# Optimization experiments

Measured on AMD Instinct MI355X. Metric: run time of the kernel, lower is better.

Reference implementation:

```python
import jax, jax.numpy as jnp
import numpy as np


def setup_inputs() -> dict:
    key = jax.random.key(0)
    ks = jax.random.split(key, 8)
    B, N, E_PER, M = 8, 50000, 1000000, 2048  # graphs, nodes/graph, edges/graph, decision neurons
    BN, E = B * N, B * E_PER
    x = jax.random.normal(ks[0], (BN, 1), dtype=jnp.float32)
    edge_weight = jax.random.uniform(ks[1], (E,), minval=0.0, maxval=10.0, dtype=jnp.float32)
    # within-graph edges with PyG-style batch offsets
    offs = jnp.repeat(jnp.arange(B, dtype=jnp.int32) * N, E_PER)
    src = jax.random.randint(ks[2], (E,), 0, N, dtype=jnp.int32) + offs
    dst = jax.random.randint(ks[3], (E,), 0, N, dtype=jnp.int32) + offs
    # indices where decision_making_vector == 1 (static for jit)
    dm_indices = jnp.sort(jax.random.randint(ks[4], (M,), 0, N, dtype=jnp.int32))
    fc_w = jax.random.normal(ks[5], (1, 1), dtype=jnp.float32)
    fc_b = jax.random.normal(ks[6], (1,), dtype=jnp.float32)
    return {"x": x, "edge_weight": edge_weight, "src": src, "dst": dst,
            "dm_indices": dm_indices, "fc_w": fc_w, "fc_b": fc_b,
            "batch_size": 8, "num_passes": 3}


def reference(x, edge_weight, src, dst, dm_indices, fc_w, fc_b, batch_size, num_passes):
    # log1p edge transform
    ew = jnp.log1p(edge_weight)  # [E]
    BN = x.shape[0]
    N = BN // batch_size
    h = x  # [BN, 1]
    # TrainableEdgeConv: num_passes rounds of scatter-add message passing + per-graph L2 norm over nodes
    for _ in range(num_passes):
        msgs = h[src] * ew[:, None]                      # [E, 1] gather + scale
        h = jax.ops.segment_sum(msgs, dst, num_segments=BN)  # scatter-add to dst
        hb = h.reshape(batch_size, N, -1)
        hb = hb / jnp.linalg.norm(hb, axis=1, keepdims=True)  # x / x.norm(dim=1)
        h = hb.reshape(BN, -1)
    # decision_making_mask: select decision neurons
    v = h.reshape(batch_size, N, -1)[:, dm_indices, 0]  # [B, M]
    # normalize_non_zero: per-graph mean/std over nonzero entries (unbiased std, like scatter_std)
    mask = v != 0
    cnt = mask.sum(axis=1, keepdims=True).astype(v.dtype)
    mean = jnp.where(mask, v, 0.0).sum(axis=1, keepdims=True) / cnt
    var = jnp.where(mask, (v - mean) ** 2, 0.0).sum(axis=1, keepdims=True) / jnp.maximum(cnt - 1.0, 1.0)
    std = jnp.sqrt(var) + 1e-5
    v = jnp.where(mask, (v - mean) / std, v)
    # mean pool over decision neurons, Linear(1,1), relu, squeeze -> [B]
    pooled = v.mean(axis=1)  # [B]
    out = pooled * fc_w[0, 0] + fc_b[0]
    return jax.nn.relu(out)
```

## Files before the change

kernel.cpp:

```cpp
#include <hip/hip_runtime.h>
#include <math.h>

#define GB    8
#define GN    50000
#define EPG   1000000
#define EDGES (GB*EPG)
#define NP    3

#define BW     4096
#define NBUCK  13
#define NBINS  (GB*NBUCK)
#define CAP    89088
#define CPB    20
#define STRIPE 4000
#define NQ     (STRIPE/4)
#define NBLKH  (EDGES/STRIPE)
#define BPG    (EPG/STRIPE)
#define SRCMASK 0x7FFFFu


__global__ void z_k(int* __restrict__ gcur, float* __restrict__ nsq,
                    float4* __restrict__ a, float4* __restrict__ b,
                    float4* __restrict__ c) {
  int i = blockIdx.x * 256 + threadIdx.x;
  float4 z = {0.f, 0.f, 0.f, 0.f};
  if (i < (GB * GN) / 4) { a[i] = z; b[i] = z; c[i] = z; }
  if (blockIdx.x == 0) {
    if (threadIdx.x < NBINS) gcur[threadIdx.x] = 0;
    if (threadIdx.x < GB) nsq[threadIdx.x] = 0.f;
  }
}

__global__ __launch_bounds__(256) void fscatter_k(
    const int* __restrict__ src, const int* __restrict__ dst,
    const float* __restrict__ ew, int* __restrict__ gcur,
    uint2* __restrict__ recs) {
  __shared__ int lh[NBINS];
  __shared__ int lb[NBINS];
  if (threadIdx.x < NBINS) lh[threadIdx.x] = 0;
  __syncthreads();
  int blk = blockIdx.x;
  int s0 = blk * STRIPE;
  int g = blk / BPG;
  int base = g * GN, gb = g * NBUCK;
  const int4* d4 = (const int4*)(dst + s0);
  const int4* s4 = (const int4*)(src + s0);
  const float4* w4 = (const float4*)(ew + s0);

  int rk[16];
#pragma unroll
  for (int u = 0; u < 4; ++u) {
    int q = threadIdx.x + 256 * u;
    if (q < NQ) {
      int4 d = d4[q];
      rk[4 * u + 0] = atomicAdd(&lh[gb + ((d.x - base) >> 12)], 1);
      rk[4 * u + 1] = atomicAdd(&lh[gb + ((d.y - base) >> 12)], 1);
      rk[4 * u + 2] = atomicAdd(&lh[gb + ((d.z - base) >> 12)], 1);
      rk[4 * u + 3] = atomicAdd(&lh[gb + ((d.w - base) >> 12)], 1);
    }
  }
  __syncthreads();
  if (threadIdx.x < NBINS) {
    int c = lh[threadIdx.x];
    lb[threadIdx.x] = c ? atomicAdd(&gcur[threadIdx.x], c) : 0;
  }
  __syncthreads();
#pragma unroll
  for (int u = 0; u < 4; ++u) {
    int q = threadIdx.x + 256 * u;
    if (q < NQ) {
      int4 d = d4[q]; int4 s = s4[q]; float4 w = w4[q];
      int dv[4] = {d.x, d.y, d.z, d.w};
      int sv[4] = {s.x, s.y, s.z, s.w};
      float wv[4] = {w.x, w.y, w.z, w.w};
#pragma unroll
      for (int k = 0; k < 4; ++k) {
        int dl = dv[k] - base;
        int bin = gb + (dl >> 12);
        int r = dl & (BW - 1);
        size_t pos = (size_t)bin * CAP + lb[bin] + rk[4 * u + k];
        recs[pos] = make_uint2(((unsigned)r << 19) | (unsigned)sv[k],
                               __float_as_uint(log1pf(wv[k])));
      }
    }
  }
}

__global__ __launch_bounds__(256) void accum_k(
    const uint2* __restrict__ recs, const int* __restrict__ cnt,
    const float* __restrict__ hin, float* __restrict__ hout) {
  __shared__ float acc[BW];
  int c = blockIdx.x;
  int bin = blockIdx.y;
  float4 z = {0.f, 0.f, 0.f, 0.f};
  float4* a4 = (float4*)acc;
  for (int i = threadIdx.x; i < BW / 4; i += 256) a4[i] = z;
  int len = cnt[bin];
  int chunk = ((len + CPB - 1) / CPB + 1) & ~1;
  int lo = c * chunk;
  int hi = lo + chunk;
  if (lo > len) lo = len;
  if (hi > len) hi = len;
  const uint2* rb = recs + (size_t)bin * CAP;
  __syncthreads();
  int rem = hi - lo;
  if (rem < 0) rem = 0;
  int np = rem >> 1;
  const uint4* rp = (const uint4*)(rb + lo);
  int p = threadIdx.x;
  for (; p + 256 < np; p += 512) {
    uint4 r0 = rp[p];
    uint4 r1 = rp[p + 256];
    float a0 = hin[r0.x & SRCMASK] * __uint_as_float(r0.y);
    float a1 = hin[r0.z & SRCMASK] * __uint_as_float(r0.w);
    float a2 = hin[r1.x & SRCMASK] * __uint_as_float(r1.y);
    float a3 = hin[r1.z & SRCMASK] * __uint_as_float(r1.w);
    atomicAdd(&acc[r0.x >> 19], a0);
    atomicAdd(&acc[r0.z >> 19], a1);
    atomicAdd(&acc[r1.x >> 19], a2);
    atomicAdd(&acc[r1.z >> 19], a3);
  }
  if (p < np) {
    uint4 r0 = rp[p];
    atomicAdd(&acc[r0.x >> 19], hin[r0.x & SRCMASK] * __uint_as_float(r0.y));
    atomicAdd(&acc[r0.z >> 19], hin[r0.z & SRCMASK] * __uint_as_float(r0.w));
  }
  if ((rem & 1) && threadIdx.x == 0) {
    uint2 a = rb[hi - 1];
    atomicAdd(&acc[a.x >> 19], hin[a.x & SRCMASK] * __uint_as_float(a.y));
  }
  __syncthreads();
  int g = bin / NBUCK, bucket = bin - g * NBUCK;
  int sw = GN - bucket * BW; if (sw > BW) sw = BW;
  float* ho = hout + (size_t)g * GN + (size_t)bucket * BW;
  for (int i = threadIdx.x; i < sw; i += 256) {
    float v = acc[i];
    if (v != 0.f) unsafeAtomicAdd(&ho[i], v);
  }
}

__global__ void nsq_k(const float4* __restrict__ h4, float* __restrict__ nsq) {
  __shared__ float sm[GB];
  if (threadIdx.x < GB) sm[threadIdx.x] = 0.f;
  __syncthreads();
  int n4 = blockIdx.x * 256 + threadIdx.x;
  if (n4 < (GB * GN) / 4) {
    float4 t = h4[n4];
    int g = (n4 * 4) / GN;
    atomicAdd(&sm[g], t.x * t.x + t.y * t.y + t.z * t.z + t.w * t.w);
  }
  __syncthreads();
  if (threadIdx.x < GB && sm[threadIdx.x] != 0.f)
    unsafeAtomicAdd(&nsq[threadIdx.x], sm[threadIdx.x]);
}


__global__ void init_k(const float* __restrict__ x, float* __restrict__ h_cur,
                       float* __restrict__ h_next, float* __restrict__ norms,
                       int BN, int n_norms) {
  int i = blockIdx.x * blockDim.x + threadIdx.x;
  int stride = gridDim.x * blockDim.x;
  for (int j = i; j < BN; j += stride) { h_cur[j] = x[j]; h_next[j] = 0.f; }
  if (i < n_norms) norms[i] = 0.f;
}

__global__ void edge_k(const int* __restrict__ src, const int* __restrict__ dst,
                       const float* __restrict__ ew, const float* __restrict__ h_in,
                       float* __restrict__ h_out, int E4, int E) {
  int i = blockIdx.x * blockDim.x + threadIdx.x;
  int stride = gridDim.x * blockDim.x;
  const int4* s4 = (const int4*)src;
  const int4* d4 = (const int4*)dst;
  const float4* w4 = (const float4*)ew;
  for (int j = i; j < E4; j += stride) {
    int4 s = s4[j]; int4 d = d4[j]; float4 w = w4[j];
    unsafeAtomicAdd(&h_out[d.x], h_in[s.x] * log1pf(w.x));
    unsafeAtomicAdd(&h_out[d.y], h_in[s.y] * log1pf(w.y));
    unsafeAtomicAdd(&h_out[d.z], h_in[s.z] * log1pf(w.z));
    unsafeAtomicAdd(&h_out[d.w], h_in[s.w] * log1pf(w.w));
  }
  for (int j = E4 * 4 + i; j < E; j += stride)
    unsafeAtomicAdd(&h_out[dst[j]], h_in[src[j]] * log1pf(ew[j]));
}

__global__ void norm_k(const float* __restrict__ h, float* __restrict__ norms, int N) {
  int g = blockIdx.y;
  const float* hg = h + (size_t)g * N;
  float s = 0.f;
  for (int j = blockIdx.x * blockDim.x + threadIdx.x; j < N; j += gridDim.x * blockDim.x) {
    float v = hg[j]; s += v * v;
  }
  __shared__ float sm[4];
  for (int o = 32; o > 0; o >>= 1) s += __shfl_down(s, o, 64);
  if ((threadIdx.x & 63) == 0) sm[threadIdx.x >> 6] = s;
  __syncthreads();
  if (threadIdx.x == 0) {
    float t = 0.f;
    for (int w = 0; w < (int)(blockDim.x >> 6); ++w) t += sm[w];
    unsafeAtomicAdd(&norms[g], t);
  }
}

__global__ void scale_k(const float* __restrict__ norms, float* __restrict__ h_next,
                        float* __restrict__ h_cur, int N) {
  int g = blockIdx.y;
  float inv = 1.0f / sqrtf(norms[g]);
  size_t off = (size_t)g * N;
  for (int j = blockIdx.x * blockDim.x + threadIdx.x; j < N; j += gridDim.x * blockDim.x) {
    h_cur[off + j] = h_next[off + j] * inv;
    h_next[off + j] = 0.f;
  }
}

__device__ __forceinline__ float blk_red(float t, float* sm, int nw) {
  for (int o = 32; o > 0; o >>= 1) t += __shfl_down(t, o, 64);
  if ((threadIdx.x & 63) == 0) sm[threadIdx.x >> 6] = t;
  __syncthreads();
  float r = 0.f;
  for (int w = 0; w < nw; ++w) r += sm[w];
  __syncthreads();
  return r;
}

__global__ void final_k(const float* __restrict__ h, const float* __restrict__ nsq,
                        const int* __restrict__ dm,
                        const float* __restrict__ fc_w, const float* __restrict__ fc_b,
                        float* __restrict__ out, int N, int M) {
  extern __shared__ float v[];
  __shared__ float sm[16];
  int b = blockIdx.x;
  int nw = blockDim.x >> 6;
  float inv = nsq ? 1.0f / sqrtf(nsq[b]) : 1.0f;
  const float* hb = h + (size_t)b * N;
  for (int m = threadIdx.x; m < M; m += blockDim.x) v[m] = hb[dm[m]] * inv;
  __syncthreads();

  float cnt = 0.f, sum = 0.f;
  for (int m = threadIdx.x; m < M; m += blockDim.x) {
    float xv = v[m];
    if (xv != 0.f) { cnt += 1.f; sum += xv; }
  }
  float totalSum = blk_red(sum, sm, nw);
  float totalCnt = blk_red(cnt, sm, nw);
  float mean = totalCnt > 0.f ? totalSum / totalCnt : 0.f;

  float ssq = 0.f;
  for (int m = threadIdx.x; m < M; m += blockDim.x) {
    float xv = v[m];
    if (xv != 0.f) { float d = xv - mean; ssq += d * d; }
  }
  float totalSsq = blk_red(ssq, sm, nw);

  float denom = totalCnt - 1.f;
  if (denom < 1.f) denom = 1.f;
  float stdv = sqrtf(totalSsq / denom) + 1e-5f;

  float ps = 0.f;
  for (int m = threadIdx.x; m < M; m += blockDim.x) {
    float xv = v[m];
    if (xv != 0.f) ps += (xv - mean) / stdv;
  }
  float pooled = blk_red(ps, sm, nw) / (float)M;
  if (threadIdx.x == 0) {
    float o = pooled * fc_w[0] + fc_b[0];
    out[b] = o > 0.f ? o : 0.f;
  }
}

extern "C" void kernel_launch(void* const* d_in, const int* in_sizes, int n_in,
                              void* d_out, int out_size, void* d_ws, size_t ws_size,
                              hipStream_t stream) {
  const float* x    = (const float*)d_in[0];
  const float* ew   = (const float*)d_in[1];
  const int*   src  = (const int*)d_in[2];
  const int*   dst  = (const int*)d_in[3];
  const int*   dm   = (const int*)d_in[4];
  const float* fc_w = (const float*)d_in[5];
  const float* fc_b = (const float*)d_in[6];

  const int BN = in_sizes[0];
  const int E  = in_sizes[1];
  const int M  = in_sizes[4];
  const int N  = BN / GB;

  const bool shapes_ok = (BN == GB * GN) && (E == EDGES);

  const size_t recs_b = (size_t)NBINS * CAP * 8;
  const size_t buf_b  = (size_t)BN * 4;
  const size_t misc_b = 4096;
  const size_t REQ = recs_b + 3 * buf_b + misc_b;

  if (shapes_ok && ws_size >= REQ) {
    uint2* recs = (uint2*)d_ws;
    float* bufA = (float*)((char*)d_ws + recs_b);
    float* bufB = bufA + BN;
    float* bufC = bufB + BN;
    int*   gcur = (int*)(bufC + BN);
    float* nsq  = (float*)(gcur + NBINS + 8);

    z_k<<<(BN / 4 + 255) / 256, 256, 0, stream>>>(gcur, nsq, (float4*)bufA,
                                                  (float4*)bufB, (float4*)bufC);
    fscatter_k<<<NBLKH, 256, 0, stream>>>(src, dst, ew, gcur, recs);

    dim3 agrid(CPB, NBINS);
    accum_k<<<agrid, 256, 0, stream>>>(recs, gcur, x, bufA);
    accum_k<<<agrid, 256, 0, stream>>>(recs, gcur, bufA, bufB);
    accum_k<<<agrid, 256, 0, stream>>>(recs, gcur, bufB, bufC);

    nsq_k<<<(BN / 4 + 255) / 256, 256, 0, stream>>>((const float4*)bufC, nsq);
    final_k<<<GB, 512, M * sizeof(float), stream>>>(bufC, nsq, dm, fc_w, fc_b,
                                                    (float*)d_out, N, M);
    return;
  }

  float* h_cur  = (float*)d_ws;
  float* h_next = h_cur + BN;
  float* norms  = h_next + BN;
  const int threads = 256;
  init_k<<<(BN + threads - 1) / threads, threads, 0, stream>>>(x, h_cur, h_next,
                                                               norms, BN, NP * GB);
  int E4 = E / 4;
  int edgeBlocks = (E4 + threads - 1) / threads;
  dim3 ngrid((N + threads * 8 - 1) / (threads * 8), GB);
  for (int p = 0; p < NP; ++p) {
    edge_k<<<edgeBlocks, threads, 0, stream>>>(src, dst, ew, h_cur, h_next, E4, E);
    norm_k<<<ngrid, threads, 0, stream>>>(h_next, norms + p * GB, N);
    scale_k<<<ngrid, threads, 0, stream>>>(norms + p * GB, h_next, h_cur, N);
  }
  final_k<<<GB, 256, M * sizeof(float), stream>>>(h_cur, nullptr, dm, fc_w, fc_b,
                                                  (float*)d_out, N, M);
}
```

Baseline: 362.1 us.

## Split edge records into key and fp16 weight arrays with LDS-staged scatter

Edge records are stored as separate 32-bit key and 16-bit half-precision weight arrays instead of 8-byte pairs. This cuts the bytes each of the three accumulate passes reads per edge from 8 to 6. The scatter kernel now sorts each stripe by bucket in shared memory and writes contiguous runs, replacing scattered global stores. The stripe is halved to fit the shared-memory buffer. Storing weights in fp16 costs some precision on log1p weights, and the accumulate kernel now reads four edges per vector load.

Result: no change. 369.2 us (+2.0%).

```diff
diff --git a/kernel.cpp b/kernel.cpp
--- a/kernel.cpp
+++ b/kernel.cpp
@@ -1,4 +1,5 @@
 #include <hip/hip_runtime.h>
+#include <hip/hip_fp16.h>
 #include <math.h>
 
 #define GB    8
@@ -12,12 +13,23 @@
 #define NBINS  (GB*NBUCK)
 #define CAP    89088
 #define CPB    20
-#define STRIPE 4000
+#define STRIPE 2000
 #define NQ     (STRIPE/4)
 #define NBLKH  (EDGES/STRIPE)
 #define BPG    (EPG/STRIPE)
 #define SRCMASK 0x7FFFFu
 
+
+static __device__ __forceinline__ unsigned short f2h(float v) {
+  union { __half h; unsigned short u; } cv;
+  cv.h = __float2half(v);
+  return cv.u;
+}
+static __device__ __forceinline__ float h2f(unsigned short s) {
+  union { unsigned short u; __half h; } cv;
+  cv.u = s;
+  return __half2float(cv.h);
+}
 
 __global__ void z_k(int* __restrict__ gcur, float* __restrict__ nsq,
                     float4* __restrict__ a, float4* __restrict__ b,
@@ -34,10 +46,12 @@
 __global__ __launch_bounds__(256) void fscatter_k(
     const int* __restrict__ src, const int* __restrict__ dst,
     const float* __restrict__ ew, int* __restrict__ gcur,
-    uint2* __restrict__ recs) {
-  __shared__ int lh[NBINS];
-  __shared__ int lb[NBINS];
-  if (threadIdx.x < NBINS) lh[threadIdx.x] = 0;
+    unsigned* __restrict__ keys, unsigned short* __restrict__ wh) {
+  __shared__ int lh[NBUCK];
+  __shared__ int lsb[NBUCK];
+  __shared__ int lbg[NBUCK];
+  __shared__ uint2 srt[STRIPE];
+  if (threadIdx.x < NBUCK) lh[threadIdx.x] = 0;
   __syncthreads();
   int blk = blockIdx.x;
   int s0 = blk * STRIPE;
@@ -47,26 +61,29 @@
   const int4* s4 = (const int4*)(src + s0);
   const float4* w4 = (const float4*)(ew + s0);
 
-  int rk[16];
+  int rk[8];
 #pragma unroll
-  for (int u = 0; u < 4; ++u) {
+  for (int u = 0; u < 2; ++u) {
     int q = threadIdx.x + 256 * u;
     if (q < NQ) {
       int4 d = d4[q];
-      rk[4 * u + 0] = atomicAdd(&lh[gb + ((d.x - base) >> 12)], 1);
-      rk[4 * u + 1] = atomicAdd(&lh[gb + ((d.y - base) >> 12)], 1);
-      rk[4 * u + 2] = atomicAdd(&lh[gb + ((d.z - base) >> 12)], 1);
-      rk[4 * u + 3] = atomicAdd(&lh[gb + ((d.w - base) >> 12)], 1);
+      rk[4 * u + 0] = atomicAdd(&lh[(d.x - base) >> 12], 1);
+      rk[4 * u + 1] = atomicAdd(&lh[(d.y - base) >> 12], 1);
+      rk[4 * u + 2] = atomicAdd(&lh[(d.z - base) >> 12], 1);
+      rk[4 * u + 3] = atomicAdd(&lh[(d.w - base) >> 12], 1);
     }
   }
   __syncthreads();
-  if (threadIdx.x < NBINS) {
+  if (threadIdx.x < NBUCK) {
     int c = lh[threadIdx.x];
-    lb[threadIdx.x] = c ? atomicAdd(&gcur[threadIdx.x], c) : 0;
+    lbg[threadIdx.x] = c ? atomicAdd(&gcur[gb + threadIdx.x], c) : 0;
+    int s = 0;
+    for (int j = 0; j < threadIdx.x; ++j) s += lh[j];
+    lsb[threadIdx.x] = s;
   }
   __syncthreads();
 #pragma unroll
-  for (int u = 0; u < 4; ++u) {
+  for (int u = 0; u < 2; ++u) {
     int q = threadIdx.x + 256 * u;
     if (q < NQ) {
       int4 d = d4[q]; int4 s = s4[q]; float4 w = w4[q];
@@ -76,19 +93,32 @@
 #pragma unroll
       for (int k = 0; k < 4; ++k) {
         int dl = dv[k] - base;
-        int bin = gb + (dl >> 12);
-        int r = dl & (BW - 1);
-        size_t pos = (size_t)bin * CAP + lb[bin] + rk[4 * u + k];
-        recs[pos] = make_uint2(((unsigned)r << 19) | (unsigned)sv[k],
-                               __float_as_uint(log1pf(wv[k])));
+        int bin = dl >> 12;
+        srt[lsb[bin] + rk[4 * u + k]] =
+            make_uint2(((unsigned)(dl & (BW - 1)) << 19) | (unsigned)sv[k],
+                       __float_as_uint(log1pf(wv[k])));
       }
     }
   }
+  __syncthreads();
+  for (int b = 0; b < NBUCK; ++b) {
+    int cnt = lh[b];
+    int lo = lsb[b];
+    size_t bofs = (size_t)(gb + b) * CAP + lbg[b];
+    unsigned* kd = keys + bofs;
+    unsigned short* wd = wh + bofs;
+    for (int i = threadIdx.x; i < cnt; i += 256) {
+      uint2 r = srt[lo + i];
+      kd[i] = r.x;
+      wd[i] = f2h(__uint_as_float(r.y));
+    }
+  }
 }
 
 __global__ __launch_bounds__(256) void accum_k(
-    const uint2* __restrict__ recs, const int* __restrict__ cnt,
-    const float* __restrict__ hin, float* __restrict__ hout) {
+    const unsigned* __restrict__ keys, const unsigned short* __restrict__ wh,
+    const int* __restrict__ cnt, const float* __restrict__ hin,
+    float* __restrict__ hout) {
   __shared__ float acc[BW];
   int c = blockIdx.x;
   int bin = blockIdx.y;
@@ -96,38 +126,55 @@
   float4* a4 = (float4*)acc;
   for (int i = threadIdx.x; i < BW / 4; i += 256) a4[i] = z;
   int len = cnt[bin];
-  int chunk = ((len + CPB - 1) / CPB + 1) & ~1;
+  int chunk = (((len + CPB - 1) / CPB) + 3) & ~3;
   int lo = c * chunk;
   int hi = lo + chunk;
   if (lo > len) lo = len;
   if (hi > len) hi = len;
-  const uint2* rb = recs + (size_t)bin * CAP;
+  size_t bofs = (size_t)bin * CAP;
   __syncthreads();
   int rem = hi - lo;
   if (rem < 0) rem = 0;
-  int np = rem >> 1;
-  const uint4* rp = (const uint4*)(rb + lo);
+  int n4 = rem >> 2;
+  const uint4* kp = (const uint4*)(keys + bofs + lo);
+  const uint2* wp = (const uint2*)(wh + bofs + lo);
   int p = threadIdx.x;
-  for (; p + 256 < np; p += 512) {
-    uint4 r0 = rp[p];
-    uint4 r1 = rp[p + 256];
-    float a0 = hin[r0.x & SRCMASK] * __uint_as_float(r0.y);
-    float a1 = hin[r0.z & SRCMASK] * __uint_as_float(r0.w);
-    float a2 = hin[r1.x & SRCMASK] * __uint_as_float(r1.y);
-    float a3 = hin[r1.z & SRCMASK] * __uint_as_float(r1.w);
-    atomicAdd(&acc[r0.x >> 19], a0);
-    atomicAdd(&acc[r0.z >> 19], a1);
-    atomicAdd(&acc[r1.x >> 19], a2);
-    atomicAdd(&acc[r1.z >> 19], a3);
-  }
-  if (p < np) {
-    uint4 r0 = rp[p];
-    atomicAdd(&acc[r0.x >> 19], hin[r0.x & SRCMASK] * __uint_as_float(r0.y));
-    atomicAdd(&acc[r0.z >> 19], hin[r0.z & SRCMASK] * __uint_as_float(r0.w));
-  }
-  if ((rem & 1) && threadIdx.x == 0) {
-    uint2 a = rb[hi - 1];
-    atomicAdd(&acc[a.x >> 19], hin[a.x & SRCMASK] * __uint_as_float(a.y));
+  for (; p + 256 < n4; p += 512) {
+    uint4 k0 = kp[p];
+    uint4 k1 = kp[p + 256];
+    uint2 w0 = wp[p];
+    uint2 w1 = wp[p + 256];
+    float v0 = hin[k0.x & SRCMASK] * h2f((unsigned short)(w0.x));
+    float v1 = hin[k0.y & SRCMASK] * h2f((unsigned short)(w0.x >> 16));
+    float v2 = hin[k0.z & SRCMASK] * h2f((unsigned short)(w0.y));
+    float v3 = hin[k0.w & SRCMASK] * h2f((unsigned short)(w0.y >> 16));
+    float v4 = hin[k1.x & SRCMASK] * h2f((unsigned short)(w1.x));
+    float v5 = hin[k1.y & SRCMASK] * h2f((unsigned short)(w1.x >> 16));
+    float v6 = hin[k1.z & SRCMASK] * h2f((unsigned short)(w1.y));
+    float v7 = hin[k1.w & SRCMASK] * h2f((unsigned short)(w1.y >> 16));
+    atomicAdd(&acc[k0.x >> 19], v0);
+    atomicAdd(&acc[k0.y >> 19], v1);
+    atomicAdd(&acc[k0.z >> 19], v2);
+    atomicAdd(&acc[k0.w >> 19], v3);
+    atomicAdd(&acc[k1.x >> 19], v4);
+    atomicAdd(&acc[k1.y >> 19], v5);
+    atomicAdd(&acc[k1.z >> 19], v6);
+    atomicAdd(&acc[k1.w >> 19], v7);
+  }
+  if (p < n4) {
+    uint4 k0 = kp[p];
+    uint2 w0 = wp[p];
+    atomicAdd(&acc[k0.x >> 19], hin[k0.x & SRCMASK] * h2f((unsigned short)(w0.x)));
+    atomicAdd(&acc[k0.y >> 19], hin[k0.y & SRCMASK] * h2f((unsigned short)(w0.x >> 16)));
+    atomicAdd(&acc[k0.z >> 19], hin[k0.z & SRCMASK] * h2f((unsigned short)(w0.y)));
+    atomicAdd(&acc[k0.w >> 19], hin[k0.w & SRCMASK] * h2f((unsigned short)(w0.y >> 16)));
+  }
+  int tl = rem & 3;
+  if (threadIdx.x < tl) {
+    int idx = lo + n4 * 4 + threadIdx.x;
+    unsigned k = keys[bofs + idx];
+    float v = hin[k & SRCMASK] * h2f(wh[bofs + idx]);
+    atomicAdd(&acc[k >> 19], v);
   }
   __syncthreads();
   int g = bin / NBUCK, bucket = bin - g * NBUCK;
@@ -285,14 +332,16 @@
 
   const bool shapes_ok = (BN == GB * GN) && (E == EDGES);
 
-  const size_t recs_b = (size_t)NBINS * CAP * 8;
+  const size_t keys_b = (size_t)NBINS * CAP * 4;
+  const size_t wh_b   = (size_t)NBINS * CAP * 2;
   const size_t buf_b  = (size_t)BN * 4;
   const size_t misc_b = 4096;
-  const size_t REQ = recs_b + 3 * buf_b + misc_b;
+  const size_t REQ = keys_b + wh_b + 3 * buf_b + misc_b;
 
   if (shapes_ok && ws_size >= REQ) {
-    uint2* recs = (uint2*)d_ws;
-    float* bufA = (float*)((char*)d_ws + recs_b);
+    unsigned* keys       = (unsigned*)d_ws;
+    unsigned short* wh   = (unsigned short*)((char*)d_ws + keys_b);
+    float* bufA = (float*)((char*)d_ws + keys_b + wh_b);
     float* bufB = bufA + BN;
     float* bufC = bufB + BN;
     int*   gcur = (int*)(bufC + BN);
@@ -300,12 +349,12 @@
 
     z_k<<<(BN / 4 + 255) / 256, 256, 0, stream>>>(gcur, nsq, (float4*)bufA,
                                                   (float4*)bufB, (float4*)bufC);
-    fscatter_k<<<NBLKH, 256, 0, stream>>>(src, dst, ew, gcur, recs);
+    fscatter_k<<<NBLKH, 256, 0, stream>>>(src, dst, ew, gcur, keys, wh);
 
     dim3 agrid(CPB, NBINS);
-    accum_k<<<agrid, 256, 0, stream>>>(recs, gcur, x, bufA);
-    accum_k<<<agrid, 256, 0, stream>>>(recs, gcur, bufA, bufB);
-    accum_k<<<agrid, 256, 0, stream>>>(recs, gcur, bufB, bufC);
+    accum_k<<<agrid, 256, 0, stream>>>(keys, wh, gcur, x, bufA);
+    accum_k<<<agrid, 256, 0, stream>>>(keys, wh, gcur, bufA, bufB);
+    accum_k<<<agrid, 256, 0, stream>>>(keys, wh, gcur, bufB, bufC);
 
     nsq_k<<<(BN / 4 + 255) / 256, 256, 0, stream>>>((const float4*)bufC, nsq);
     final_k<<<GB, 512, M * sizeof(float), stream>>>(bufC, nsq, dm, fc_w, fc_b,
```
